# Performance work log

Measured on AMD Instinct MI355X. Metric: run time of the kernel, lower is better.

## Reference

```python
import jax, jax.numpy as jnp
import numpy as np

N = 50000
E = 1600000
IN_CH = 64


def _sage_conv(x, edge_index, W_l, b_l, W_r):
    # PyG SAGEConv with mean aggregation:
    #   out = lin_l(mean_{j in N(i)} x_j) + lin_r(x_i)
    src, dst = edge_index[0], edge_index[1]
    n = x.shape[0]
    msg_sum = jax.ops.segment_sum(x[src], dst, num_segments=n)          # [N, d_in]
    cnt = jax.ops.segment_sum(jnp.ones((src.shape[0],), x.dtype), dst,
                              num_segments=n)                            # [N]
    agg = msg_sum / jnp.maximum(cnt, 1.0)[:, None]                       # mean, 0 if no nbrs
    return agg @ W_l.T + b_l + x @ W_r.T


def setup_inputs() -> dict:
    key = jax.random.key(0)
    ks = jax.random.split(key, 9)
    x = jax.random.normal(ks[0], (N, IN_CH), dtype=jnp.float32)
    edge_index = jax.random.randint(ks[1], (2, E), 0, N, dtype=jnp.int64)
    s = 1.0 / np.sqrt(IN_CH)
    W1_l = jax.random.uniform(ks[2], (64, IN_CH), jnp.float32, -s, s)
    b1_l = jnp.zeros((64,), jnp.float32)
    W1_r = jax.random.uniform(ks[3], (64, IN_CH), jnp.float32, -s, s)
    s2 = 1.0 / np.sqrt(64)
    W2_l = jax.random.uniform(ks[4], (32, 64), jnp.float32, -s2, s2)
    b2_l = jnp.zeros((32,), jnp.float32)
    W2_r = jax.random.uniform(ks[5], (32, 64), jnp.float32, -s2, s2)
    s3 = 1.0 / np.sqrt(32)
    W_lin = jax.random.uniform(ks[6], (1, 32), jnp.float32, -s3, s3)
    b_lin = jax.random.uniform(ks[7], (1,), jnp.float32, -s3, s3)
    return {"x": x, "edge_index": edge_index,
            "W1_l": W1_l, "b1_l": b1_l, "W1_r": W1_r,
            "W2_l": W2_l, "b2_l": b2_l, "W2_r": W2_r,
            "W_lin": W_lin, "b_lin": b_lin}


def reference(x, edge_index, W1_l, b1_l, W1_r, W2_l, b2_l, W2_r, W_lin, b_lin):
    h = jax.nn.relu(_sage_conv(x, edge_index, W1_l, b1_l, W1_r))   # [N, 64]
    h = jax.nn.relu(_sage_conv(h, edge_index, W2_l, b2_l, W2_r))   # [N, 32]
    return h @ W_lin.T + b_lin                                      # [N, 1]
```

## Files before the change

kernel.cpp:

```cpp
#include <hip/hip_runtime.h>
#include <cstdint>
#include <cstddef>

using u8  = unsigned char;
using u16 = unsigned short;
using u32 = unsigned int;

typedef short short8 __attribute__((ext_vector_type(8)));
typedef float f32x4 __attribute__((ext_vector_type(4)));

#define NB 256
#define HCAP4 12544

__device__ __forceinline__ float bf2f(u16 h) { return __uint_as_float(((u32)h) << 16); }
__device__ __forceinline__ u16 f2bf(float f) {
    u32 u = __float_as_uint(f);
    u += 0x7FFFu + ((u >> 16) & 1u);
    return (u16)(u >> 16);
}

__device__ __forceinline__ void load8(const float* p, float* v) {
    float4 a = ((const float4*)p)[0];
    float4 b = ((const float4*)p)[1];
    v[0]=a.x; v[1]=a.y; v[2]=a.z; v[3]=a.w;
    v[4]=b.x; v[5]=b.y; v[6]=b.z; v[7]=b.w;
}
__device__ __forceinline__ void load8(const u16* p, float* v) {
    uint4 u = *(const uint4*)p;
    v[0]=__uint_as_float(u.x << 16); v[1]=__uint_as_float(u.x & 0xFFFF0000u);
    v[2]=__uint_as_float(u.y << 16); v[3]=__uint_as_float(u.y & 0xFFFF0000u);
    v[4]=__uint_as_float(u.z << 16); v[5]=__uint_as_float(u.z & 0xFFFF0000u);
    v[6]=__uint_as_float(u.w << 16); v[7]=__uint_as_float(u.w & 0xFFFF0000u);
}
__device__ __forceinline__ void store8bf(u16* p, const float* v) {
    uint4 w;
    w.x = (u32)f2bf(v[0]) | ((u32)f2bf(v[1]) << 16);
    w.y = (u32)f2bf(v[2]) | ((u32)f2bf(v[3]) << 16);
    w.z = (u32)f2bf(v[4]) | ((u32)f2bf(v[5]) << 16);
    w.w = (u32)f2bf(v[6]) | ((u32)f2bf(v[7]) << 16);
    *(uint4*)p = w;
}
__device__ __forceinline__ short8 ld8b(const u16* p) {
    union { uint4 u; short8 s; } c;
    c.u = *(const uint4*)p;
    return c.s;
}

__global__ __launch_bounds__(256) void split_x_kernel(const float* __restrict__ x,
                                                      u16* __restrict__ xh,
                                                      u16* __restrict__ xl, int total8) {
    const int c = blockIdx.x * blockDim.x + threadIdx.x;
    if (c >= total8) return;
    float v[8], lo[8];
    load8(x + (size_t)c * 8, v);
    #pragma unroll
    for (int k = 0; k < 8; ++k) lo[k] = v[k] - bf2f(f2bf(v[k]));
    store8bf(xh + (size_t)c * 8, v);
    store8bf(xl + (size_t)c * 8, lo);
}

__global__ __launch_bounds__(1024) void hist_lds_kernel(const int* idx,
                                                        u32* __restrict__ mat,
                                                        u8* __restrict__ within,
                                                        u32* __restrict__ pe, int E, int n) {
    __shared__ u32 h[HCAP4];
    __shared__ int s_nz;
    const int t = threadIdx.x;
    const int hw4 = (n + 3) >> 2;
    if (t == 0) s_nz = 0;
    for (int w = t; w < hw4; w += 1024) h[w] = 0;
    if (t < 128 && ((const u32*)idx)[2 * t + 1] != 0u) atomicOr(&s_nz, 1);
    __syncthreads();
    const int stride = s_nz ? 1 : 2;
    const int chunk = (E + NB - 1) / NB;
    const int b = blockIdx.x;
    const int e1 = min(b * chunk + chunk, E);
    for (int e = b * chunk + t; e < e1; e += 1024) {
        const int s = idx[(size_t)e * stride];
        const int d = idx[(size_t)(E + e) * stride];
        const int sh = (d & 3) << 3;
        const u32 old = atomicAdd(&h[d >> 2], 1u << sh);
        within[e] = (u8)((old >> sh) & 0xFFu);
        pe[e] = ((u32)d << 16) | (u32)s;
    }
    __syncthreads();
    u32* dst = mat + (size_t)b * hw4;
    for (int w = t; w < hw4; w += 1024) dst[w] = h[w];
}

__global__ __launch_bounds__(256) void csr_base_kernel(u32* __restrict__ mat,
                                                       int* __restrict__ deg, int n) {
    __shared__ u32 gs[16][17];
    const int hw4 = (n + 3) >> 2;
    const int wl = threadIdx.x & 15;
    const int j  = threadIdx.x >> 4;
    const int w = blockIdx.x * 16 + wl;
    u32 c[16];
    u32 s = 0;
    if (w < hw4) {
        #pragma unroll
        for (int k = 0; k < 16; ++k) {
            c[k] = mat[(size_t)(j * 16 + k) * hw4 + w];
            s += c[k];
        }
    }
    gs[j][wl] = s;
    __syncthreads();
    u32 run = 0, total = 0;
    for (int g = 0; g < 16; ++g) {
        const u32 v = gs[g][wl];
        if (g < j) run += v;
        total += v;
    }
    if (w < hw4) {
        #pragma unroll
        for (int k = 0; k < 16; ++k) {
            const size_t o = (size_t)(j * 16 + k) * hw4 + w;
            const u32 v = c[k];
            mat[o] = run;
            run += v;
        }
        if (j == 0) {
            #pragma unroll
            for (int q = 0; q < 4; ++q) {
                const int node = 4 * w + q;
                if (node < n) deg[node] = (int)((total >> (q << 3)) & 0xFFu);
            }
        }
    }
}

__global__ __launch_bounds__(256) void scan_partials_kernel(const int* __restrict__ deg,
                                                            int* __restrict__ bsum, int n) {
    __shared__ int ws[4];
    const int i = blockIdx.x * 256 + threadIdx.x;
    int v = (i < n) ? deg[i] : 0;
    #pragma unroll
    for (int m = 1; m < 64; m <<= 1) v += __shfl_xor(v, m, 64);
    const int lane = threadIdx.x & 63, wv = threadIdx.x >> 6;
    if (lane == 0) ws[wv] = v;
    __syncthreads();
    if (threadIdx.x == 0) bsum[blockIdx.x] = ws[0] + ws[1] + ws[2] + ws[3];
}
__global__ __launch_bounds__(256) void scan_bsums_kernel(const int* __restrict__ bsum,
                                                         int* __restrict__ boff, int nb) {
    __shared__ int ws[4];
    const int t = threadIdx.x;
    const int lane = t & 63, wv = t >> 6;
    int x = (t < nb) ? bsum[t] : 0;
    int v = x;
    #pragma unroll
    for (int o = 1; o < 64; o <<= 1) {
        int u = __shfl_up(v, o, 64);
        if (lane >= o) v += u;
    }
    if (lane == 63) ws[wv] = v;
    __syncthreads();
    int woff = 0;
    for (int w = 0; w < wv; ++w) woff += ws[w];
    if (t < nb) boff[t] = v + woff - x;
}
__global__ __launch_bounds__(256) void scan_write_kernel(const int* __restrict__ deg,
                                                         const int* __restrict__ boff,
                                                         int* __restrict__ row_ptr, int n) {
    __shared__ int ws[4];
    const int t = threadIdx.x;
    const int i = blockIdx.x * 256 + t;
    const int lane = t & 63, wv = t >> 6;
    const int x = (i < n) ? deg[i] : 0;
    int v = x;
    #pragma unroll
    for (int o = 1; o < 64; o <<= 1) {
        int u = __shfl_up(v, o, 64);
        if (lane >= o) v += u;
    }
    if (lane == 63) ws[wv] = v;
    __syncthreads();
    int woff = boff[blockIdx.x];
    for (int w = 0; w < wv; ++w) woff += ws[w];
    const int excl = v - x + woff;
    if (i < n) row_ptr[i] = excl;
    if (i == n - 1) row_ptr[n] = excl + x;
}

__global__ __launch_bounds__(1024) void scatter_kernel(const u32* __restrict__ pe,
                                                       const u32* __restrict__ mat,
                                                       const int* __restrict__ row_ptr,
                                                       const u8* __restrict__ within,
                                                       u16* __restrict__ ssrc, int E, int n) {
    const int hw4 = (n + 3) >> 2;
    const int chunk = (E + NB - 1) / NB;
    const int b = blockIdx.x;
    const int e1 = min(b * chunk + chunk, E);
    const u32* base = mat + (size_t)b * hw4;
    for (int e = b * chunk + threadIdx.x; e < e1; e += 1024) {
        const u32 p = pe[e];
        const int s = (int)(p & 0xFFFFu);
        const int d = (int)(p >> 16);
        const int wb = (int)((base[d >> 2] >> ((d & 3) << 3)) & 0xFFu);
        ssrc[row_ptr[d] + wb + (int)within[e]] = (u16)s;
    }
}

__global__ __launch_bounds__(256) void agg64_kernel(const u16* __restrict__ feat,
                                                    const int* __restrict__ row_ptr,
                                                    const u16* __restrict__ ssrc,
                                                    u16* __restrict__ out, int n) {
    const int lane = threadIdx.x & 63;
    const int wid = (blockIdx.x * blockDim.x + threadIdx.x) >> 6;
    const int nw = (gridDim.x * blockDim.x) >> 6;
    const int g = lane >> 3;
    const int q = lane & 7;
    for (int i = wid; i < n; i += nw) {
        const int rb = row_ptr[i], re = row_ptr[i + 1];
        float acc[8];
        #pragma unroll
        for (int k = 0; k < 8; ++k) acc[k] = 0.f;
        for (int e = rb + g; e < re; e += 8) {
            int s = (int)ssrc[e];
            float v[8];
            load8(feat + (size_t)s * 64 + q * 8, v);
            #pragma unroll
            for (int k = 0; k < 8; ++k) acc[k] += v[k];
        }
        #pragma unroll
        for (int m = 8; m < 64; m <<= 1) {
            #pragma unroll
            for (int k = 0; k < 8; ++k) acc[k] += __shfl_xor(acc[k], m, 64);
        }
        if (g == 0) {
            float inv = 1.0f / (float)max(re - rb, 1);
            #pragma unroll
            for (int k = 0; k < 8; ++k) acc[k] *= inv;
            store8bf(out + (size_t)i * 64 + q * 8, acc);
        }
    }
}

#define W1P 140
#define W2P 76
__global__ __launch_bounds__(256) void layer1_mfma_kernel(
    const u16* __restrict__ A1b, const u16* __restrict__ xh, const u16* __restrict__ xl,
    const float* __restrict__ W1l, const float* __restrict__ b1,
    const float* __restrict__ W1r, const float* __restrict__ W2l,
    const float* __restrict__ b2, const float* __restrict__ W2r,
    u16* __restrict__ z2, float* __restrict__ r2, int n)
{
    __shared__ alignas(16) u16 w1h[64 * W1P], w1l[64 * W1P];
    __shared__ alignas(16) u16 w2h[64 * W2P], w2l[64 * W2P];
    __shared__ alignas(16) u16 h1h[64 * W2P], h1l[64 * W2P];

    const int t = threadIdx.x;
    for (int c = t; c < 64 * 32; c += 256) {
        const int ch = c >> 5, k = (c & 31) * 4;
        const float* src = (k < 64) ? (W1l + ch * 64 + k) : (W1r + ch * 64 + (k - 64));
        float4 w = *(const float4*)src;
        const float wv[4] = {w.x, w.y, w.z, w.w};
        #pragma unroll
        for (int j = 0; j < 4; ++j) {
            u16 h = f2bf(wv[j]);
            w1h[ch * W1P + k + j] = h;
            w1l[ch * W1P + k + j] = f2bf(wv[j] - bf2f(h));
        }
    }
    for (int c = t; c < 64 * 16; c += 256) {
        const int ch = c >> 4, k = (c & 15) * 4;
        const float* src = (ch < 32) ? (W2l + ch * 64 + k) : (W2r + (ch - 32) * 64 + k);
        float4 w = *(const float4*)src;
        const float wv[4] = {w.x, w.y, w.z, w.w};
        #pragma unroll
        for (int j = 0; j < 4; ++j) {
            u16 h = f2bf(wv[j]);
            w2h[ch * W2P + k + j] = h;
            w2l[ch * W2P + k + j] = f2bf(wv[j] - bf2f(h));
        }
    }
    __syncthreads();

    const int lane = t & 63;
    const int wv = t >> 6;
    const int m = lane & 15, quad = lane >> 4;
    const int base = blockIdx.x * 64 + wv * 16;

    const int nodeA = min(base + m, n - 1);
    const u16* a1row = A1b + (size_t)nodeA * 64;
    const u16* xhrow = xh + (size_t)nodeA * 64;
    const u16* xlrow = xl + (size_t)nodeA * 64;
    short8 aA[2], aH[2], aL[2];
    aA[0] = ld8b(a1row + quad * 8);      aA[1] = ld8b(a1row + 32 + quad * 8);
    aH[0] = ld8b(xhrow + quad * 8);      aH[1] = ld8b(xhrow + 32 + quad * 8);
    aL[0] = ld8b(xlrow + quad * 8);      aL[1] = ld8b(xlrow + 32 + quad * 8);

    #pragma unroll
    for (int ni = 0; ni < 4; ++ni) {
        const int row = ni * 16 + m;
        f32x4 acc = {0.f, 0.f, 0.f, 0.f};
        #pragma unroll
        for (int kc = 0; kc < 2; ++kc) {
            short8 b = ld8b(&w1h[row * W1P + kc * 32 + quad * 8]);
            acc = __builtin_amdgcn_mfma_f32_16x16x32_bf16(aA[kc], b, acc, 0, 0, 0);
        }
        #pragma unroll
        for (int kc = 0; kc < 2; ++kc) {
            short8 bh = ld8b(&w1h[row * W1P + 64 + kc * 32 + quad * 8]);
            short8 bl = ld8b(&w1l[row * W1P + 64 + kc * 32 + quad * 8]);
            acc = __builtin_amdgcn_mfma_f32_16x16x32_bf16(aH[kc], bh, acc, 0, 0, 0);
            acc = __builtin_amdgcn_mfma_f32_16x16x32_bf16(aH[kc], bl, acc, 0, 0, 0);
            acc = __builtin_amdgcn_mfma_f32_16x16x32_bf16(aL[kc], bh, acc, 0, 0, 0);
        }
        const float bias = b1[row];
        #pragma unroll
        for (int r = 0; r < 4; ++r) {
            float h = fmaxf(acc[r] + bias, 0.0f);
            u16 hh = f2bf(h);
            h1h[(wv * 16 + quad * 4 + r) * W2P + row] = hh;
            h1l[(wv * 16 + quad * 4 + r) * W2P + row] = f2bf(h - bf2f(hh));
        }
    }

    short8 ah[2], al[2];
    ah[0] = ld8b(&h1h[(wv * 16 + m) * W2P + quad * 8]);
    ah[1] = ld8b(&h1h[(wv * 16 + m) * W2P + 32 + quad * 8]);
    al[0] = ld8b(&h1l[(wv * 16 + m) * W2P + quad * 8]);
    al[1] = ld8b(&h1l[(wv * 16 + m) * W2P + 32 + quad * 8]);

    #pragma unroll
    for (int ni = 0; ni < 4; ++ni) {
        const int row = ni * 16 + m;
        f32x4 acc = {0.f, 0.f, 0.f, 0.f};
        #pragma unroll
        for (int kc = 0; kc < 2; ++kc) {
            short8 bh = ld8b(&w2h[row * W2P + kc * 32 + quad * 8]);
            short8 bl = ld8b(&w2l[row * W2P + kc * 32 + quad * 8]);
            acc = __builtin_amdgcn_mfma_f32_16x16x32_bf16(ah[kc], bh, acc, 0, 0, 0);
            acc = __builtin_amdgcn_mfma_f32_16x16x32_bf16(ah[kc], bl, acc, 0, 0, 0);
            acc = __builtin_amdgcn_mfma_f32_16x16x32_bf16(al[kc], bh, acc, 0, 0, 0);
        }
        if (ni < 2) {
            #pragma unroll
            for (int r = 0; r < 4; ++r) {
                int node = base + quad * 4 + r;
                if (node < n) z2[(size_t)node * 32 + row] = f2bf(acc[r]);
            }
        } else {
            const int ch = row - 32;
            const float bias = b2[ch];
            #pragma unroll
            for (int r = 0; r < 4; ++r) {
                int node = base + quad * 4 + r;
                if (node < n) r2[(size_t)node * 32 + ch] = acc[r] + bias;
            }
        }
    }
}

__global__ __launch_bounds__(256) void layer2_final_kernel(
    const u16* __restrict__ z2, const float* __restrict__ r2,
    const int* __restrict__ row_ptr, const u16* __restrict__ ssrc,
    const float* __restrict__ Wlin, const float* __restrict__ blin,
    float* __restrict__ out, int n)
{
    const int lane = threadIdx.x & 63;
    const int wid = (blockIdx.x * blockDim.x + threadIdx.x) >> 6;
    const int nw = (gridDim.x * blockDim.x) >> 6;
    const int g = lane >> 2;
    const int q = lane & 3;
    float wlin8[8];
    load8(Wlin + q * 8, wlin8);
    const float bl = blin[0];
    for (int i = wid; i < n; i += nw) {
        const int rb = row_ptr[i], re = row_ptr[i + 1];
        float acc[8];
        #pragma unroll
        for (int k = 0; k < 8; ++k) acc[k] = 0.f;
        for (int e = rb + g; e < re; e += 16) {
            int s = (int)ssrc[e];
            float v[8];
            load8(z2 + (size_t)s * 32 + q * 8, v);
            #pragma unroll
            for (int k = 0; k < 8; ++k) acc[k] += v[k];
        }
        #pragma unroll
        for (int m = 4; m < 64; m <<= 1) {
            #pragma unroll
            for (int k = 0; k < 8; ++k) acc[k] += __shfl_xor(acc[k], m, 64);
        }
        float partial = 0.0f;
        if (g == 0) {
            const float inv = 1.0f / (float)max(re - rb, 1);
            float r2v[8];
            load8(r2 + (size_t)i * 32 + q * 8, r2v);
            #pragma unroll
            for (int k = 0; k < 8; ++k)
                partial += fmaxf(fmaf(acc[k], inv, r2v[k]), 0.0f) * wlin8[k];
        }
        partial += __shfl_xor(partial, 1, 64);
        partial += __shfl_xor(partial, 2, 64);
        if (lane == 0) out[i] = partial + bl;
    }
}

extern "C" void kernel_launch(void* const* d_in, const int* in_sizes, int n_in,
                              void* d_out, int out_size, void* d_ws, size_t ws_size,
                              hipStream_t stream) {
    (void)n_in; (void)out_size; (void)ws_size;
    const int N = in_sizes[0] / 64;
    const int E = in_sizes[1] / 2;
    const int hw4 = (N + 3) >> 2;

    char* ws = (char*)d_ws;
    size_t off = 0;
    auto alloc = [&](size_t bytes) -> void* {
        void* p = ws + off;
        off += (bytes + 255) & ~(size_t)255;
        return p;
    };
    u32*   mat     = (u32*)alloc((size_t)NB * hw4 * 4);
    u8*    within  = (u8*)alloc((size_t)E);
    u32*   pe      = (u32*)alloc((size_t)E * 4);
    int*   deg     = (int*)alloc((size_t)N * 4);
    int*   row_ptr = (int*)alloc(((size_t)N + 1) * 4);
    u16*   ssrc    = (u16*)alloc((size_t)E * 2);
    int*   bsum    = (int*)alloc(1024);
    int*   boff    = (int*)alloc(1024);
    u16*   xh      = (u16*)alloc((size_t)N * 64 * 2);
    u16*   xl      = (u16*)alloc((size_t)N * 64 * 2);
    u16*   A1b     = (u16*)alloc((size_t)N * 64 * 2);
    u16*   z2      = (u16*)alloc((size_t)N * 32 * 2);
    float* r2      = (float*)alloc((size_t)N * 32 * 4);

    const int* idx = (const int*)d_in[1];
    const int nb2 = (N + 255) / 256;

    split_x_kernel<<<(N * 8 + 255) / 256, 256, 0, stream>>>((const float*)d_in[0], xh, xl, N * 8);

    hist_lds_kernel<<<NB, 1024, 0, stream>>>(idx, mat, within, pe, E, N);
    csr_base_kernel<<<(hw4 + 15) / 16, 256, 0, stream>>>(mat, deg, N);
    scan_partials_kernel<<<nb2, 256, 0, stream>>>(deg, bsum, N);
    scan_bsums_kernel<<<1, 256, 0, stream>>>(bsum, boff, nb2);
    scan_write_kernel<<<nb2, 256, 0, stream>>>(deg, boff, row_ptr, N);
    scatter_kernel<<<NB, 1024, 0, stream>>>(pe, mat, row_ptr, within, ssrc, E, N);

    agg64_kernel<<<2048, 256, 0, stream>>>(xh, row_ptr, ssrc, A1b, N);

    layer1_mfma_kernel<<<(N + 63) / 64, 256, 0, stream>>>(A1b, xh, xl,
        (const float*)d_in[2], (const float*)d_in[3], (const float*)d_in[4],
        (const float*)d_in[5], (const float*)d_in[6], (const float*)d_in[7],
        z2, r2, N);

    layer2_final_kernel<<<2048, 256, 0, stream>>>(z2, r2, row_ptr, ssrc,
        (const float*)d_in[8], (const float*)d_in[9], (float*)d_out, N);
}
```

Measured before the change: 227.4 us.

## Fuse x split into histogram kernel, merge scan stages, unroll gather loops

Moves the fp32-to-bf16 hi/lo split of x into the histogram kernel, so each block converts a slice of x alongside its edge chunk. The separate block-sum scan kernel is removed: each scan_write block now reduces the preceding block sums itself. Together this drops two kernel launches and the boff buffer. The two neighbor-aggregation loops now use two independent accumulators and issue two gathers per iteration to get more memory-level parallelism, at the cost of extra registers.

Result: faster. 220.9 us (-2.9%).

```diff
diff --git a/kernel.cpp b/kernel.cpp
--- a/kernel.cpp
+++ b/kernel.cpp
@@ -46,34 +46,38 @@
     return c.s;
 }
 
-__global__ __launch_bounds__(256) void split_x_kernel(const float* __restrict__ x,
-                                                      u16* __restrict__ xh,
-                                                      u16* __restrict__ xl, int total8) {
-    const int c = blockIdx.x * blockDim.x + threadIdx.x;
-    if (c >= total8) return;
-    float v[8], lo[8];
-    load8(x + (size_t)c * 8, v);
-    #pragma unroll
-    for (int k = 0; k < 8; ++k) lo[k] = v[k] - bf2f(f2bf(v[k]));
-    store8bf(xh + (size_t)c * 8, v);
-    store8bf(xl + (size_t)c * 8, lo);
-}
-
 __global__ __launch_bounds__(1024) void hist_lds_kernel(const int* idx,
+                                                        const float* __restrict__ x,
+                                                        u16* __restrict__ xh,
+                                                        u16* __restrict__ xl,
                                                         u32* __restrict__ mat,
                                                         u8* __restrict__ within,
-                                                        u32* __restrict__ pe, int E, int n) {
+                                                        u32* __restrict__ pe,
+                                                        int E, int n, int total8) {
     __shared__ u32 h[HCAP4];
     __shared__ int s_nz;
     const int t = threadIdx.x;
+    const int b = blockIdx.x;
     const int hw4 = (n + 3) >> 2;
     if (t == 0) s_nz = 0;
     for (int w = t; w < hw4; w += 1024) h[w] = 0;
     if (t < 128 && ((const u32*)idx)[2 * t + 1] != 0u) atomicOr(&s_nz, 1);
+
+    {
+        const int nt = (total8 + NB - 1) / NB;
+        const int c1 = min(b * nt + nt, total8);
+        for (int c = b * nt + t; c < c1; c += 1024) {
+            float v[8], lo[8];
+            load8(x + (size_t)c * 8, v);
+            #pragma unroll
+            for (int k = 0; k < 8; ++k) lo[k] = v[k] - bf2f(f2bf(v[k]));
+            store8bf(xh + (size_t)c * 8, v);
+            store8bf(xl + (size_t)c * 8, lo);
+        }
+    }
     __syncthreads();
     const int stride = s_nz ? 1 : 2;
     const int chunk = (E + NB - 1) / NB;
-    const int b = blockIdx.x;
     const int e1 = min(b * chunk + chunk, E);
     for (int e = b * chunk + t; e < e1; e += 1024) {
         const int s = idx[(size_t)e * stride];
@@ -142,31 +146,23 @@
     __syncthreads();
     if (threadIdx.x == 0) bsum[blockIdx.x] = ws[0] + ws[1] + ws[2] + ws[3];
 }
-__global__ __launch_bounds__(256) void scan_bsums_kernel(const int* __restrict__ bsum,
-                                                         int* __restrict__ boff, int nb) {
+
+__global__ __launch_bounds__(256) void scan_write_kernel(const int* __restrict__ deg,
+                                                         const int* __restrict__ bsum,
+                                                         int* __restrict__ row_ptr,
+                                                         int n, int nb) {
+    __shared__ int wr[4];
     __shared__ int ws[4];
+    __shared__ int s_boff;
     const int t = threadIdx.x;
     const int lane = t & 63, wv = t >> 6;
-    int x = (t < nb) ? bsum[t] : 0;
-    int v = x;
+    int pv = (t < nb && t < blockIdx.x) ? bsum[t] : 0;
     #pragma unroll
-    for (int o = 1; o < 64; o <<= 1) {
-        int u = __shfl_up(v, o, 64);
-        if (lane >= o) v += u;
-    }
-    if (lane == 63) ws[wv] = v;
-    __syncthreads();
-    int woff = 0;
-    for (int w = 0; w < wv; ++w) woff += ws[w];
-    if (t < nb) boff[t] = v + woff - x;
-}
-__global__ __launch_bounds__(256) void scan_write_kernel(const int* __restrict__ deg,
-                                                         const int* __restrict__ boff,
-                                                         int* __restrict__ row_ptr, int n) {
-    __shared__ int ws[4];
-    const int t = threadIdx.x;
+    for (int o = 1; o < 64; o <<= 1) pv += __shfl_xor(pv, o, 64);
+    if (lane == 0) wr[wv] = pv;
+    __syncthreads();
+    if (t == 0) s_boff = wr[0] + wr[1] + wr[2] + wr[3];
     const int i = blockIdx.x * 256 + t;
-    const int lane = t & 63, wv = t >> 6;
     const int x = (i < n) ? deg[i] : 0;
     int v = x;
     #pragma unroll
@@ -176,7 +172,7 @@
     }
     if (lane == 63) ws[wv] = v;
     __syncthreads();
-    int woff = boff[blockIdx.x];
+    int woff = s_boff;
     for (int w = 0; w < wv; ++w) woff += ws[w];
     const int excl = v - x + woff;
     if (i < n) row_ptr[i] = excl;
@@ -213,26 +209,38 @@
     const int q = lane & 7;
     for (int i = wid; i < n; i += nw) {
         const int rb = row_ptr[i], re = row_ptr[i + 1];
-        float acc[8];
-        #pragma unroll
-        for (int k = 0; k < 8; ++k) acc[k] = 0.f;
-        for (int e = rb + g; e < re; e += 8) {
-            int s = (int)ssrc[e];
-            float v[8];
-            load8(feat + (size_t)s * 64 + q * 8, v);
-            #pragma unroll
-            for (int k = 0; k < 8; ++k) acc[k] += v[k];
-        }
+        float acc0[8], acc1[8];
+        #pragma unroll
+        for (int k = 0; k < 8; ++k) { acc0[k] = 0.f; acc1[k] = 0.f; }
+        int e = rb + g;
+        for (; e + 8 < re; e += 16) {
+            const int s0 = (int)ssrc[e];
+            const int s1 = (int)ssrc[e + 8];
+            float v0[8], v1[8];
+            load8(feat + (size_t)s0 * 64 + q * 8, v0);
+            load8(feat + (size_t)s1 * 64 + q * 8, v1);
+            #pragma unroll
+            for (int k = 0; k < 8; ++k) { acc0[k] += v0[k]; acc1[k] += v1[k]; }
+        }
+        if (e < re) {
+            const int s0 = (int)ssrc[e];
+            float v0[8];
+            load8(feat + (size_t)s0 * 64 + q * 8, v0);
+            #pragma unroll
+            for (int k = 0; k < 8; ++k) acc0[k] += v0[k];
+        }
+        #pragma unroll
+        for (int k = 0; k < 8; ++k) acc0[k] += acc1[k];
         #pragma unroll
         for (int m = 8; m < 64; m <<= 1) {
             #pragma unroll
-            for (int k = 0; k < 8; ++k) acc[k] += __shfl_xor(acc[k], m, 64);
+            for (int k = 0; k < 8; ++k) acc0[k] += __shfl_xor(acc0[k], m, 64);
         }
         if (g == 0) {
             float inv = 1.0f / (float)max(re - rb, 1);
             #pragma unroll
-            for (int k = 0; k < 8; ++k) acc[k] *= inv;
-            store8bf(out + (size_t)i * 64 + q * 8, acc);
+            for (int k = 0; k < 8; ++k) acc0[k] *= inv;
+            store8bf(out + (size_t)i * 64 + q * 8, acc0);
         }
     }
 }
@@ -370,20 +378,32 @@
     const float bl = blin[0];
     for (int i = wid; i < n; i += nw) {
         const int rb = row_ptr[i], re = row_ptr[i + 1];
-        float acc[8];
-        #pragma unroll
-        for (int k = 0; k < 8; ++k) acc[k] = 0.f;
-        for (int e = rb + g; e < re; e += 16) {
-            int s = (int)ssrc[e];
-            float v[8];
-            load8(z2 + (size_t)s * 32 + q * 8, v);
-            #pragma unroll
-            for (int k = 0; k < 8; ++k) acc[k] += v[k];
-        }
+        float acc0[8], acc1[8];
+        #pragma unroll
+        for (int k = 0; k < 8; ++k) { acc0[k] = 0.f; acc1[k] = 0.f; }
+        int e = rb + g;
+        for (; e + 16 < re; e += 32) {
+            const int s0 = (int)ssrc[e];
+            const int s1 = (int)ssrc[e + 16];
+            float v0[8], v1[8];
+            load8(z2 + (size_t)s0 * 32 + q * 8, v0);
+            load8(z2 + (size_t)s1 * 32 + q * 8, v1);
+            #pragma unroll
+            for (int k = 0; k < 8; ++k) { acc0[k] += v0[k]; acc1[k] += v1[k]; }
+        }
+        if (e < re) {
+            const int s0 = (int)ssrc[e];
+            float v0[8];
+            load8(z2 + (size_t)s0 * 32 + q * 8, v0);
+            #pragma unroll
+            for (int k = 0; k < 8; ++k) acc0[k] += v0[k];
+        }
+        #pragma unroll
+        for (int k = 0; k < 8; ++k) acc0[k] += acc1[k];
         #pragma unroll
         for (int m = 4; m < 64; m <<= 1) {
             #pragma unroll
-            for (int k = 0; k < 8; ++k) acc[k] += __shfl_xor(acc[k], m, 64);
+            for (int k = 0; k < 8; ++k) acc0[k] += __shfl_xor(acc0[k], m, 64);
         }
         float partial = 0.0f;
         if (g == 0) {
@@ -392,7 +412,7 @@
             load8(r2 + (size_t)i * 32 + q * 8, r2v);
             #pragma unroll
             for (int k = 0; k < 8; ++k)
-                partial += fmaxf(fmaf(acc[k], inv, r2v[k]), 0.0f) * wlin8[k];
+                partial += fmaxf(fmaf(acc0[k], inv, r2v[k]), 0.0f) * wlin8[k];
         }
         partial += __shfl_xor(partial, 1, 64);
         partial += __shfl_xor(partial, 2, 64);
@@ -422,7 +442,6 @@
     int*   row_ptr = (int*)alloc(((size_t)N + 1) * 4);
     u16*   ssrc    = (u16*)alloc((size_t)E * 2);
     int*   bsum    = (int*)alloc(1024);
-    int*   boff    = (int*)alloc(1024);
     u16*   xh      = (u16*)alloc((size_t)N * 64 * 2);
     u16*   xl      = (u16*)alloc((size_t)N * 64 * 2);
     u16*   A1b     = (u16*)alloc((size_t)N * 64 * 2);
@@ -432,13 +451,11 @@
     const int* idx = (const int*)d_in[1];
     const int nb2 = (N + 255) / 256;
 
-    split_x_kernel<<<(N * 8 + 255) / 256, 256, 0, stream>>>((const float*)d_in[0], xh, xl, N * 8);
-
-    hist_lds_kernel<<<NB, 1024, 0, stream>>>(idx, mat, within, pe, E, N);
+    hist_lds_kernel<<<NB, 1024, 0, stream>>>(idx, (const float*)d_in[0], xh, xl,
+                                             mat, within, pe, E, N, N * 8);
     csr_base_kernel<<<(hw4 + 15) / 16, 256, 0, stream>>>(mat, deg, N);
     scan_partials_kernel<<<nb2, 256, 0, stream>>>(deg, bsum, N);
-    scan_bsums_kernel<<<1, 256, 0, stream>>>(bsum, boff, nb2);
-    scan_write_kernel<<<nb2, 256, 0, stream>>>(deg, boff, row_ptr, N);
+    scan_write_kernel<<<nb2, 256, 0, stream>>>(deg, bsum, row_ptr, N, nb2);
     scatter_kernel<<<NB, 1024, 0, stream>>>(pe, mat, row_ptr, within, ssrc, E, N);
 
     agg64_kernel<<<2048, 256, 0, stream>>>(xh, row_ptr, ssrc, A1b, N);
```
